# Kernel optimization log

Measured on AMD Instinct MI355X. Metric: run time of the kernel, lower is better.

## Reference

```python
import jax, jax.numpy as jnp
import numpy as np

PAD_IND = 3
SOS_IND = 0
NSTEPS = 25
H = 256   # hidden_size
D = 256   # input_size (embedding dim)
L = 3     # lstm_layers


def _lstm_cell(x, h, c, Wih, Whh, bih, bhh):
    # torch LSTM gate order: i, f, g, o
    g = x @ Wih.T + bih + h @ Whh.T + bhh
    i, f, gg, o = jnp.split(g, 4, axis=-1)
    c2 = jax.nn.sigmoid(f) * c + jax.nn.sigmoid(i) * jnp.tanh(gg)
    h2 = jax.nn.sigmoid(o) * jnp.tanh(c2)
    return h2, c2


def setup_inputs() -> dict:
    key = jax.random.key(0)
    ks = jax.random.split(key, 24)
    B, T = 64, 256
    Vin, C = 32000, 32000
    s = 1.0 / np.sqrt(H)

    def u(k, shape):
        return jax.random.uniform(k, shape, jnp.float32, -s, s)

    return dict(
        x=jax.random.randint(ks[0], (B, T), 0, Vin),
        target_val=jax.random.randint(ks[1], (B, NSTEPS), 0, C),
        enc_embed=jax.random.normal(ks[2], (Vin, D), jnp.float32),
        enc_Wih=u(ks[3], (L, 4 * H, D)),
        enc_Whh=u(ks[4], (L, 4 * H, H)),
        enc_bih=u(ks[5], (L, 4 * H)),
        enc_bhh=u(ks[6], (L, 4 * H)),
        Wq=u(ks[7], (H, H)), bq=u(ks[8], (H,)),
        Wk=u(ks[9], (H, H)), bk=u(ks[10], (H,)),
        Wv=u(ks[11], (H, H)), bv=u(ks[12], (H,)),
        Wo=u(ks[13], (H, H)), bo=u(ks[14], (H,)),
        dec_embed=jax.random.normal(ks[15], (C, D), jnp.float32),
        dec_Wih0=u(ks[16], (4 * H, 2 * H)),            # decoder layer 0 input is [emb; ctx] = 2H
        dec_Wih_rest=u(ks[17], (L - 1, 4 * H, H)),
        dec_Whh=u(ks[18], (L, 4 * H, H)),
        dec_bih=u(ks[19], (L, 4 * H)),
        dec_bhh=u(ks[20], (L, 4 * H)),
        dec_W=u(ks[21], (C, H)),
        dec_b=u(ks[22], (C,)),
    )


def reference(x, target_val, enc_embed, enc_Wih, enc_Whh, enc_bih, enc_bhh,
              Wq, bq, Wk, bk, Wv, bv, Wo, bo,
              dec_embed, dec_Wih0, dec_Wih_rest, dec_Whh, dec_bih, dec_bhh,
              dec_W, dec_b):
    B, T = x.shape
    lengths = (x != PAD_IND).sum(axis=1)            # [B], emulates pack_padded_sequence
    emb = enc_embed[x]                              # [B,T,D]
    valid = (jnp.arange(T)[:, None] < lengths[None, :])[..., None]  # [T,B,1]
    h0 = jnp.zeros((L, B, H), emb.dtype)
    c0 = jnp.zeros((L, B, H), emb.dtype)

    def enc_step(carry, inp):
        h, c = carry
        xt, v = inp
        hs, cs = [], []
        z = xt
        for l in range(L):
            hl, cl = _lstm_cell(z, h[l], c[l], enc_Wih[l], enc_Whh[l], enc_bih[l], enc_bhh[l])
            hl = jnp.where(v, hl, h[l])             # freeze state past sequence length
            cl = jnp.where(v, cl, c[l])
            hs.append(hl); cs.append(cl)
            z = hl
        h = jnp.stack(hs); c = jnp.stack(cs)
        return (h, c), jnp.where(v, h[-1], 0.0)     # pad_packed pads with zeros

    (enc_h, enc_c), outs = jax.lax.scan(enc_step, (h0, c0), (jnp.swapaxes(emb, 0, 1), valid))
    enc_hiddens = jnp.swapaxes(outs, 0, 1)          # [B,T,H]

    # attention key/value projections are loop-invariant -> hoist out of decode loop
    kp = enc_hiddens @ Wk.T + bk                    # [B,T,H]
    vp = enc_hiddens @ Wv.T + bv                    # [B,T,H]
    scale = 1.0 / jnp.sqrt(jnp.asarray(H, emb.dtype))
    dec_Wih = [dec_Wih0, dec_Wih_rest[0], dec_Wih_rest[1]]
    tok0 = jnp.full((B,), SOS_IND, jnp.int32)

    def dec_step(carry, _):
        h, c, tok = carry
        e = dec_embed[tok]                          # [B,D]
        q = h.sum(axis=0) @ Wq.T + bq               # prev_state[0].sum(axis=0) -> [B,H]
        scores = jnp.einsum('bh,bth->bt', q, kp) * scale
        attn = jax.nn.softmax(scores, axis=-1)
        ctx = jnp.einsum('bt,bth->bh', attn, vp) @ Wo.T + bo
        z = jnp.concatenate([e, ctx], axis=-1)      # [B,2H]
        hs, cs = [], []
        for l in range(L):
            hl, cl = _lstm_cell(z, h[l], c[l], dec_Wih[l], dec_Whh[l], dec_bih[l], dec_bhh[l])
            hs.append(hl); cs.append(cl)
            z = hl
        h = jnp.stack(hs); c = jnp.stack(cs)
        logits = z @ dec_W.T + dec_b                # [B,C]
        tok = jnp.argmax(logits, axis=-1).astype(jnp.int32)  # greedy feedback (TF ratio = 0)
        return (h, c, tok), logits

    _, logits = jax.lax.scan(dec_step, (enc_h, enc_c, tok0), None, length=NSTEPS)  # [25,B,C]
    return jnp.swapaxes(logits, 0, 1)[:, :, None, :]  # [B,25,1,C] like the torch module
```

## Files before the change

kernel.cpp:

```cpp
#include <hip/hip_runtime.h>
#include <math.h>

#define TT    256
#define NB    64
#define HH    256
#define NSTEP 25
#define NCLS  32000
#define PADI  3

__device__ __align__(16) float g_hring[3][2][NB][HH];
__device__ __align__(16) float g_enchid[TT][NB][HH];
__device__ __align__(16) float g_kp[NB][TT][HH];
__device__ __align__(16) float g_vp[NB][TT][HH];
__device__ __align__(16) float g_cfin[3][NB][HH];
__device__ __align__(16) float g_hdec[2][3][NB][HH];
__device__ __align__(16) float g_z0[NB][512];
__device__ float    g_wmax[256][NB];
__device__ int      g_wmaxi[256][NB];
__device__ int      g_len[NB];
__device__ unsigned g_arrive[256];
__device__ unsigned g_rel[256];

__global__ void k_zero_flags(){
  g_arrive[threadIdx.x] = 0u;
  g_rel[threadIdx.x] = 0u;
}

__device__ __forceinline__ float sigf(float v){ return 1.0f / (1.0f + expf(-v)); }

#define SCOPE_AG __HIP_MEMORY_SCOPE_AGENT
typedef unsigned long long u64;
__device__ __forceinline__ float2 ld2(const float* p){
  u64 v = __hip_atomic_load((const u64*)p, __ATOMIC_RELAXED, SCOPE_AG);
  float2 r; __builtin_memcpy(&r, &v, 8); return r;
}
__device__ __forceinline__ float ldc(const float* p){ return __hip_atomic_load(p, __ATOMIC_RELAXED, SCOPE_AG); }
__device__ __forceinline__ void  stc(float* p, float v){ __hip_atomic_store(p, v, __ATOMIC_RELAXED, SCOPE_AG); }
__device__ __forceinline__ int   ldi(const int* p){ return __hip_atomic_load(p, __ATOMIC_RELAXED, SCOPE_AG); }
__device__ __forceinline__ void  sti(int* p, int v){ __hip_atomic_store(p, v, __ATOMIC_RELAXED, SCOPE_AG); }
__device__ __forceinline__ unsigned ldu(const unsigned* p){ return __hip_atomic_load(p, __ATOMIC_RELAXED, SCOPE_AG); }
__device__ __forceinline__ void  stu(unsigned* p, unsigned v){ __hip_atomic_store(p, v, __ATOMIC_RELAXED, SCOPE_AG); }

#define DOT4(a_, x_, w_) (a_) += (x_).x*(w_).x + (x_).y*(w_).y + (x_).z*(w_).z + (x_).w*(w_).w

#define WENC(cb,g,jj,u) (((((cb)*12+(g))*8+(jj))*36)+(u))

__device__ __forceinline__ void gbar(int w, unsigned target){
  asm volatile("s_waitcnt vmcnt(0)" ::: "memory");
  __syncthreads();
  if (threadIdx.x == 0) stu(&g_arrive[w], target);
  if (w == 0){
    if (threadIdx.x < 64){
      const int i4 = threadIdx.x * 4;
      for (;;){
        unsigned a0 = ldu(&g_arrive[i4+0]);
        unsigned a1 = ldu(&g_arrive[i4+1]);
        unsigned a2 = ldu(&g_arrive[i4+2]);
        unsigned a3 = ldu(&g_arrive[i4+3]);
        if (__all((a0>=target) && (a1>=target) && (a2>=target) && (a3>=target))) break;
        __builtin_amdgcn_s_sleep(1);
      }
      if (threadIdx.x < 16) stu(&g_rel[threadIdx.x << 4], target);
    }
  } else {
    if (threadIdx.x == 0){
      const unsigned* line = &g_rel[(w >> 4) << 4];
      while (ldu(line) < target) __builtin_amdgcn_s_sleep(1);
    }
  }
  __syncthreads();
}

template<int NCB, int BASE>
__device__ __forceinline__ void dec_gates(const float* sw, const float* i0, const float* i1,
                                          const float* i2, int j, float out4[4]){
  float a0=0.f, a1=0.f, a2=0.f, a3=0.f;
  const float* ips[3] = { i0, i1, i2 };
  #pragma unroll
  for (int cb = 0; cb < NCB; ++cb){
    float2 xin[16];
    #pragma unroll
    for (int u = 0; u < 16; ++u) xin[u] = ld2(ips[cb] + u*16 + 2*j);
    #pragma unroll
    for (int u2 = 0; u2 < 8; ++u2){
      float2 pa = xin[2*u2], pb = xin[2*u2+1];
      const float* wb = &sw[BASE + (((cb*4+0)*8+j)*36) + u2*4];
      float4 w0 = *(const float4*)(wb);
      float4 w1 = *(const float4*)(wb + 288);
      float4 w2 = *(const float4*)(wb + 576);
      float4 w3 = *(const float4*)(wb + 864);
      a0 += pa.x*w0.x + pa.y*w0.y + pb.x*w0.z + pb.y*w0.w;
      a1 += pa.x*w1.x + pa.y*w1.y + pb.x*w1.z + pb.y*w1.w;
      a2 += pa.x*w2.x + pa.y*w2.y + pb.x*w2.z + pb.y*w2.w;
      a3 += pa.x*w3.x + pa.y*w3.y + pb.x*w3.z + pb.y*w3.w;
    }
  }
  #pragma unroll
  for (int m = 1; m < 8; m <<= 1){
    a0 += __shfl_xor(a0, m); a1 += __shfl_xor(a1, m);
    a2 += __shfl_xor(a2, m); a3 += __shfl_xor(a3, m);
  }
  out4[0]=a0; out4[1]=a1; out4[2]=a2; out4[3]=a3;
}

__global__ void __launch_bounds__(512, 1)
k_main(const int*   __restrict__ p_x,
       const float* __restrict__ p_eemb,
       const float* __restrict__ p_eWih,  const float* __restrict__ p_eWhh,
       const float* __restrict__ p_ebih,  const float* __restrict__ p_ebhh,
       const float* __restrict__ p_Wq, const float* __restrict__ p_bq,
       const float* __restrict__ p_Wk, const float* __restrict__ p_bk,
       const float* __restrict__ p_Wv, const float* __restrict__ p_bv,
       const float* __restrict__ p_Wo, const float* __restrict__ p_bo,
       const float* __restrict__ p_demb,
       const float* __restrict__ p_dWih0, const float* __restrict__ p_dWihR,
       const float* __restrict__ p_dWhh,
       const float* __restrict__ p_dbih,  const float* __restrict__ p_dbhh,
       const float* __restrict__ p_dW,    const float* __restrict__ p_db,
       float* __restrict__ p_out)
{
  __shared__ __align__(16) float s_w[8064];
  __shared__ __align__(16) float s_h2[NB*HH];
  __shared__ float s_benc[12];
  __shared__ float s_bdec[12];
  __shared__ __align__(16) float s_hs[256];
  __shared__ __align__(16) float s_q[256];
  __shared__ __align__(16) float s_sc[256];
  __shared__ __align__(16) float s_at[256];
  __shared__ __align__(16) float s_ctx[256];
  __shared__ float s_rv[8];  __shared__ int s_ri[8];

  const int w   = blockIdx.x;
  const int tid = threadIdx.x;
  const int b   = tid >> 3;
  const int j   = tid & 7;
  unsigned bar  = 0;

  const int lay0 = (w < 255) ? (w / 85) : 0;
  const int h0   = (w < 255) ? ((w - lay0*85) * 3) : 0;

  for (int fi = tid; fi < 6144; fi += 512){
    int g = fi >> 9, k = fi & 511;
    int e = g >> 2, gt = g & 3;
    int l   = (w < 255) ? lay0 : e;
    int hh2 = (w < 255) ? (h0 + e) : 255;
    int row = gt*256 + hh2;
    float v = (k < 256) ? p_eWih[((size_t)l*1024 + row)*256 + k]
                        : p_eWhh[((size_t)l*1024 + row)*256 + (k - 256)];
    int cb = k >> 8, kk = k & 255;
    s_w[WENC(cb, g, (kk & 15) >> 1, ((kk >> 4) << 1) | (kk & 1))] = v;
  }
  if (tid < 12){
    int e = tid >> 2, gt = tid & 3;
    int l   = (w < 255) ? lay0 : e;
    int hh2 = (w < 255) ? (h0 + e) : 255;
    int row = gt*256 + hh2;
    s_benc[tid] = p_ebih[l*1024 + row] + p_ebhh[l*1024 + row];
  }
  if (w < 64){
    int cnt = 0;
    if (tid < 256) cnt = (p_x[w*TT + tid] != PADI) ? 1 : 0;
    #pragma unroll
    for (int m = 1; m < 64; m <<= 1) cnt += __shfl_xor(cnt, m);
    if ((tid & 63) == 0) s_ri[tid >> 6] = cnt;
    __syncthreads();
    if (tid == 0){ int t2 = 0; for (int q2 = 0; q2 < 8; ++q2) t2 += s_ri[q2]; sti(&g_len[w], t2); }
  }
  if (tid < 192){
    int fi = w*192 + tid;
    int l = fi >> 14, rem = fi & 16383;
    stc(&g_hring[l][1][rem >> 8][rem & 255], 0.f);
  }
  gbar(w, ++bar);

  const int len_b = ldi(&g_len[b]);

  float c_reg[3] = {0.f,0.f,0.f};
  float h_reg[3] = {0.f,0.f,0.f};

  for (int sdiag = 0; sdiag < TT + 2; ++sdiag){
    float acc[12];
    #pragma unroll
    for (int g = 0; g < 12; ++g) acc[g] = 0.f;

    if (w < 255){
      const int t = sdiag - lay0;
      if (t >= 0 && t < TT){
        float2 x2[16], h2[16];
        if (lay0 == 0){
          const float* xs = p_eemb + (size_t)p_x[b*TT + t]*HH;
          #pragma unroll
          for (int u = 0; u < 16; ++u) x2[u] = *(const float2*)(xs + u*16 + 2*j);
        } else {
          const float* xs = &g_hring[lay0-1][t & 1][b][0];
          #pragma unroll
          for (int u = 0; u < 16; ++u) x2[u] = ld2(xs + u*16 + 2*j);
        }
        {
          const float* hsv = &g_hring[lay0][(t & 1) ^ 1][b][0];
          #pragma unroll
          for (int u = 0; u < 16; ++u) h2[u] = ld2(hsv + u*16 + 2*j);
        }
        #pragma unroll
        for (int u2 = 0; u2 < 8; ++u2){
          float2 xa = x2[2*u2], xb = x2[2*u2+1];
          float2 ha = h2[2*u2], hb = h2[2*u2+1];
          #pragma unroll
          for (int g = 0; g < 12; ++g){
            float4 wx = *(const float4*)&s_w[WENC(0, g, j, u2*4)];
            float4 wh = *(const float4*)&s_w[WENC(1, g, j, u2*4)];
            acc[g] += xa.x*wx.x + xa.y*wx.y + xb.x*wx.z + xb.y*wx.w
                    + ha.x*wh.x + ha.y*wh.y + hb.x*wh.z + hb.y*wh.w;
          }
        }
      }
    } else {
      #pragma unroll
      for (int e = 0; e < 3; ++e){
        const int t = sdiag - e;
        if (t >= 0 && t < TT){
          float2 x2[16], h2[16];
          if (e == 0){
            const float* xs = p_eemb + (size_t)p_x[b*TT + t]*HH;
            #pragma unroll
            for (int u = 0; u < 16; ++u) x2[u] = *(const float2*)(xs + u*16 + 2*j);
          } else {
            const float* xs = &g_hring[e-1][t & 1][b][0];
            #pragma unroll
            for (int u = 0; u < 16; ++u) x2[u] = ld2(xs + u*16 + 2*j);
          }
          {
            const float* hsv = &g_hring[e][(t & 1) ^ 1][b][0];
            #pragma unroll
            for (int u = 0; u < 16; ++u) h2[u] = ld2(hsv + u*16 + 2*j);
          }
          #pragma unroll
          for (int u2 = 0; u2 < 8; ++u2){
            float2 xa = x2[2*u2], xb = x2[2*u2+1];
            float2 ha = h2[2*u2], hb = h2[2*u2+1];
            #pragma unroll
            for (int g2 = 0; g2 < 4; ++g2){
              float4 wx = *(const float4*)&s_w[WENC(0, e*4+g2, j, u2*4)];
              float4 wh = *(const float4*)&s_w[WENC(1, e*4+g2, j, u2*4)];
              acc[e*4+g2] += xa.x*wx.x + xa.y*wx.y + xb.x*wx.z + xb.y*wx.w
                           + ha.x*wh.x + ha.y*wh.y + hb.x*wh.z + hb.y*wh.w;
            }
          }
        }
      }
    }

    #pragma unroll
    for (int g = 0; g < 12; ++g){
      float v = acc[g];
      v += __shfl_xor(v, 1); v += __shfl_xor(v, 2); v += __shfl_xor(v, 4);
      acc[g] = v;
    }

    if (j == 0){
      #pragma unroll
      for (int e = 0; e < 3; ++e){
        const int lay = (w < 255) ? lay0 : e;
        const int hh2 = (w < 255) ? (h0 + e) : 255;
        const int t = sdiag - lay;
        if (t >= 0 && t < TT){
          float iv = acc[e*4+0] + s_benc[e*4+0];
          float fv = acc[e*4+1] + s_benc[e*4+1];
          float gv = acc[e*4+2] + s_benc[e*4+2];
          float ov = acc[e*4+3] + s_benc[e*4+3];
          float c2 = sigf(fv)*c_reg[e] + sigf(iv)*tanhf(gv);
          float h2v = sigf(ov)*tanhf(c2);
          bool valid = (t < len_b);
          if (valid){ c_reg[e] = c2; h_reg[e] = h2v; }
          stc(&g_hring[lay][t & 1][b][hh2], h_reg[e]);
          if (lay == 2) stc(&g_enchid[t][b][hh2], valid ? h_reg[e] : 0.f);
        }
      }
    }
    gbar(w, ++bar);
  }

  if (j == 0){
    #pragma unroll
    for (int e = 0; e < 3; ++e){
      const int lay = (w < 255) ? lay0 : e;
      const int hh2 = (w < 255) ? (h0 + e) : 255;
      stc(&g_cfin[lay][b][hh2], c_reg[e]);
    }
  }
  gbar(w, ++bar);

  {
    const int b3 = w >> 2, t0 = (w & 3) * 64;
    const int n1 = tid & 127, rq = tid >> 7;
    for (int p = 0; p < 4; ++p){
      const int n = p*128 + n1;
      const float* wrow = (n < 256) ? (p_Wk + (size_t)n*HH) : (p_Wv + (size_t)(n-256)*HH);
      const float bias  = (n < 256) ? p_bk[n] : p_bv[n-256];
      const float4* wr4 = (const float4*)wrow;
      const float* hb = &g_enchid[t0 + rq*16][b3][0];
      const float4* hr[16];
      #pragma unroll
      for (int r = 0; r < 16; ++r) hr[r] = (const float4*)(hb + (size_t)r*NB*HH);
      float a16[16];
      #pragma unroll
      for (int r = 0; r < 16; ++r) a16[r] = 0.f;
      for (int k4 = 0; k4 < 64; ++k4){
        float4 wv = wr4[k4];
        #pragma unroll
        for (int r = 0; r < 16; ++r){ float4 h4 = hr[r][k4]; DOT4(a16[r], h4, wv); }
      }
      float* orow = (n < 256) ? &g_kp[b3][t0 + rq*16][n] : &g_vp[b3][t0 + rq*16][n-256];
      #pragma unroll
      for (int r = 0; r < 16; ++r) stc(orow + (size_t)r*HH, a16[r] + bias);
    }
  }

  for (int fi = tid; fi < 3072; fi += 512){
    int g = fi / 768, k = fi % 768; int row = g*256 + w;
    float v = (k < 512) ? p_dWih0[(size_t)row*512 + k]
                        : p_dWhh[(size_t)row*HH + (k - 512)];
    int cb = k >> 8, kk = k & 255;
    s_w[(((cb*4 + g)*8 + ((kk & 15) >> 1))*36) + (((kk >> 4) << 1) | (kk & 1))] = v;
  }
  for (int fi = tid; fi < 2048; fi += 512){
    int g = fi / 512, k = fi % 512; int row = g*256 + w;
    float v = (k < 256) ? p_dWihR[(size_t)row*HH + k]
                        : p_dWhh[(size_t)(1024 + row)*HH + (k - 256)];
    int cb = k >> 8, kk = k & 255;
    s_w[3456 + (((cb*4 + g)*8 + ((kk & 15) >> 1))*36) + (((kk >> 4) << 1) | (kk & 1))] = v;
  }
  for (int fi = tid; fi < 2048; fi += 512){
    int g = fi / 512, k = fi % 512; int row = g*256 + w;
    float v = (k < 256) ? p_dWihR[(size_t)(1024 + row)*HH + k]
                        : p_dWhh[(size_t)(2048 + row)*HH + (k - 256)];
    int cb = k >> 8, kk = k & 255;
    s_w[5760 + (((cb*4 + g)*8 + ((kk & 15) >> 1))*36) + (((kk >> 4) << 1) | (kk & 1))] = v;
  }
  if (tid < 12){
    int l = tid >> 2, g = tid & 3; int row = g*256 + w;
    s_bdec[tid] = p_dbih[l*1024 + row] + p_dbhh[l*1024 + row];
  }
  gbar(w, ++bar);

  if (tid < 192){
    int fi = w*192 + tid;
    int l = fi >> 14, rem = fi & 16383;
    stc(&g_hdec[0][l][rem >> 8][rem & 255], ldc(&g_hring[l][1][rem >> 8][rem & 255]));
  }
  float c_d0 = 0.f, c_d1 = 0.f, c_d2 = 0.f;
  if (j == 0){
    c_d0 = ldc(&g_cfin[0][b][w]); c_d1 = ldc(&g_cfin[1][b][w]); c_d2 = ldc(&g_cfin[2][b][w]);
  }
  gbar(w, ++bar);

  for (int st = 0; st < NSTEP; ++st){
    const int slot = st & 1, nxt = slot ^ 1;

    if (w < 64){
      const int bA = w;
      int tok = 0;
      if (st > 0){
        float v = -1e38f; int idx = 0;
        if (tid < 256){ v = ldc(&g_wmax[tid][bA]); idx = ldi(&g_wmaxi[tid][bA]); }
        #pragma unroll
        for (int m = 1; m < 64; m <<= 1){
          float ov = __shfl_xor(v, m); int oi = __shfl_xor(idx, m);
          if (ov > v || (ov == v && oi < idx)){ v = ov; idx = oi; }
        }
        if ((tid & 63) == 0){ s_rv[tid >> 6] = v; s_ri[tid >> 6] = idx; }
        __syncthreads();
        if (tid == 0){
          float bv2 = s_rv[0]; int bi2 = s_ri[0];
          for (int q2 = 1; q2 < 8; ++q2){
            float ov = s_rv[q2]; int oi = s_ri[q2];
            if (ov > bv2 || (ov == bv2 && oi < bi2)){ bv2 = ov; bi2 = oi; }
          }
          s_ri[0] = bi2;
        }
        __syncthreads();
        tok = s_ri[0];
      }
      if (tid < 256)
        s_hs[tid] = ldc(&g_hdec[slot][0][bA][tid]) + ldc(&g_hdec[slot][1][bA][tid])
                  + ldc(&g_hdec[slot][2][bA][tid]);
      __syncthreads();
      if (tid < 256){
        float a = p_bq[tid];
        const float4* wr = (const float4*)(p_Wq + (size_t)tid*HH);
        #pragma unroll 8
        for (int k4 = 0; k4 < 64; ++k4){
          float4 wv = wr[k4]; float4 h4 = *(const float4*)&s_hs[k4*4]; DOT4(a, h4, wv);
        }
        s_q[tid] = a;
      }
      __syncthreads();
      if (tid < 256){
        float a = 0.f;
        const float4* kr = (const float4*)&g_kp[bA][tid][0];
        #pragma unroll 8
        for (int k4 = 0; k4 < 64; ++k4){
          float4 kv = kr[k4]; float4 q4 = *(const float4*)&s_q[k4*4]; DOT4(a, q4, kv);
        }
        s_sc[tid] = a * 0.0625f;
      }
      __syncthreads();
      {
        float sv = (tid < 256) ? s_sc[tid] : -1e38f;
        float m2 = sv;
        #pragma unroll
        for (int m = 1; m < 64; m <<= 1) m2 = fmaxf(m2, __shfl_xor(m2, m));
        if ((tid & 63) == 0) s_rv[tid >> 6] = m2;
        __syncthreads();
        if (tid == 0){ float mm = s_rv[0]; for (int q2 = 1; q2 < 8; ++q2) mm = fmaxf(mm, s_rv[q2]); s_rv[0] = mm; }
        __syncthreads();
        const float mx = s_rv[0];
        float ev = (tid < 256) ? expf(sv - mx) : 0.f;
        float ss = ev;
        #pragma unroll
        for (int m = 1; m < 64; m <<= 1) ss += __shfl_xor(ss, m);
        __syncthreads();
        if ((tid & 63) == 0) s_rv[tid >> 6] = ss;
        __syncthreads();
        if (tid == 0){ float t2 = 0.f; for (int q2 = 0; q2 < 8; ++q2) t2 += s_rv[q2]; s_rv[0] = t2; }
        __syncthreads();
        if (tid < 256) s_at[tid] = ev / s_rv[0];
      }
      __syncthreads();
      if (tid < 256){
        float a = 0.f;
        const float* vb = &g_vp[bA][0][tid];
        #pragma unroll 4
        for (int t4 = 0; t4 < 64; ++t4){
          float4 a4 = *(const float4*)&s_at[t4*4];
          a += a4.x*vb[(size_t)(t4*4+0)*HH] + a4.y*vb[(size_t)(t4*4+1)*HH]
             + a4.z*vb[(size_t)(t4*4+2)*HH] + a4.w*vb[(size_t)(t4*4+3)*HH];
        }
        s_ctx[tid] = a;
      }
      __syncthreads();
      if (tid < 256){
        float a = p_bo[tid];
        const float4* wr = (const float4*)(p_Wo + (size_t)tid*HH);
        #pragma unroll 8
        for (int k4 = 0; k4 < 64; ++k4){
          float4 wv = wr[k4]; float4 c4 = *(const float4*)&s_ctx[k4*4]; DOT4(a, c4, wv);
        }
        stc(&g_z0[bA][256 + tid], a);
        stc(&g_z0[bA][tid], p_demb[(size_t)tok*HH + tid]);
      }
    }
    gbar(w, ++bar);

    {
      float g4[4];
      dec_gates<3, 0>(s_w, &g_z0[b][0], &g_z0[b][256], &g_hdec[slot][0][b][0], j, g4);
      if (j == 0){
        float iv = g4[0]+s_bdec[0], fv = g4[1]+s_bdec[1], gv = g4[2]+s_bdec[2], ov = g4[3]+s_bdec[3];
        float c2 = sigf(fv)*c_d0 + sigf(iv)*tanhf(gv); c_d0 = c2;
        stc(&g_hdec[nxt][0][b][w], sigf(ov)*tanhf(c2));
      }
    }
    gbar(w, ++bar);
    {
      float g4[4];
      dec_gates<2, 3456>(s_w, &g_hdec[nxt][0][b][0], &g_hdec[slot][1][b][0], nullptr, j, g4);
      if (j == 0){
        float iv = g4[0]+s_bdec[4], fv = g4[1]+s_bdec[5], gv = g4[2]+s_bdec[6], ov = g4[3]+s_bdec[7];
        float c2 = sigf(fv)*c_d1 + sigf(iv)*tanhf(gv); c_d1 = c2;
        stc(&g_hdec[nxt][1][b][w], sigf(ov)*tanhf(c2));
      }
    }
    gbar(w, ++bar);
    {
      float g4[4];
      dec_gates<2, 5760>(s_w, &g_hdec[nxt][1][b][0], &g_hdec[slot][2][b][0], nullptr, j, g4);
      if (j == 0){
        float iv = g4[0]+s_bdec[8], fv = g4[1]+s_bdec[9], gv = g4[2]+s_bdec[10], ov = g4[3]+s_bdec[11];
        float c2 = sigf(fv)*c_d2 + sigf(iv)*tanhf(gv); c_d2 = c2;
        stc(&g_hdec[nxt][2][b][w], sigf(ov)*tanhf(c2));
      }
    }
    gbar(w, ++bar);

    {
      {
        const float* src = &g_hdec[nxt][2][0][0];
        #pragma unroll
        for (int u = 0; u < 16; ++u){
          int fo = 2*(tid + 512*u);
          float2 v = ld2(src + fo);
          *(float2*)(s_h2 + fo) = v;
        }
      }
      __syncthreads();

      const int cs = tid & 63, qb = tid >> 6;
      const bool ok0 = (2*cs)   < 125;
      const bool ok1 = (2*cs+1) < 125;
      const int c0 = w*125 + 2*cs, c1 = c0 + 1;
      const float4* wr0 = (const float4*)(p_dW + (size_t)(ok0 ? c0 : w*125)*HH);
      const float4* wr1 = (const float4*)(p_dW + (size_t)(ok1 ? c1 : w*125)*HH);
      const float4* zr[8];
      #pragma unroll
      for (int r = 0; r < 8; ++r) zr[r] = (const float4*)&s_h2[(qb*8 + r)*HH];
      float a0[8], a1[8];
      #pragma unroll
      for (int r = 0; r < 8; ++r){ a0[r] = 0.f; a1[r] = 0.f; }
      for (int k4 = 0; k4 < 64; ++k4){
        float4 w0 = wr0[k4], w1 = wr1[k4];
        #pragma unroll
        for (int r = 0; r < 8; ++r){
          float4 z4 = zr[r][k4];
          DOT4(a0[r], z4, w0);
          DOT4(a1[r], z4, w1);
        }
      }
      const float bias0 = ok0 ? p_db[c0] : 0.f;
      const float bias1 = ok1 ? p_db[c1] : 0.f;
      #pragma unroll
      for (int r = 0; r < 8; ++r){
        const int bb = qb*8 + r;
        float val0 = a0[r] + bias0, val1 = a1[r] + bias1;
        float* orow = p_out + ((size_t)bb*NSTEP + st)*NCLS;
        if (ok0) orow[c0] = val0;
        if (ok1) orow[c1] = val1;
        float v = ok0 ? val0 : -1e38f;
        int idx  = ok0 ? c0 : 0x7fffffff;
        if (ok1 && val1 > v){ v = val1; idx = c1; }
        #pragma unroll
        for (int m = 1; m < 64; m <<= 1){
          float ov = __shfl_xor(v, m); int oi = __shfl_xor(idx, m);
          if (ov > v || (ov == v && oi < idx)){ v = ov; idx = oi; }
        }
        if (cs == 0){ stc(&g_wmax[w][bb], v); sti(&g_wmaxi[w][bb], idx); }
      }
    }
    gbar(w, ++bar);
  }
}

extern "C" void kernel_launch(void* const* d_in, const int* in_sizes, int n_in,
                              void* d_out, int out_size, void* d_ws, size_t ws_size,
                              hipStream_t stream){
  (void)in_sizes; (void)n_in; (void)out_size; (void)d_ws; (void)ws_size;
  const int*   x     = (const int*)d_in[0];
  const float* eemb  = (const float*)d_in[2];
  const float* eWih  = (const float*)d_in[3];
  const float* eWhh  = (const float*)d_in[4];
  const float* ebih  = (const float*)d_in[5];
  const float* ebhh  = (const float*)d_in[6];
  const float* Wq    = (const float*)d_in[7];
  const float* bq    = (const float*)d_in[8];
  const float* Wk    = (const float*)d_in[9];
  const float* bk    = (const float*)d_in[10];
  const float* Wv    = (const float*)d_in[11];
  const float* bv    = (const float*)d_in[12];
  const float* Wo    = (const float*)d_in[13];
  const float* bo    = (const float*)d_in[14];
  const float* demb  = (const float*)d_in[15];
  const float* dWih0 = (const float*)d_in[16];
  const float* dWihR = (const float*)d_in[17];
  const float* dWhh  = (const float*)d_in[18];
  const float* dbih  = (const float*)d_in[19];
  const float* dbhh  = (const float*)d_in[20];
  const float* dW    = (const float*)d_in[21];
  const float* db    = (const float*)d_in[22];
  float* out = (float*)d_out;

  k_zero_flags<<<dim3(1), dim3(256), 0, stream>>>();
  k_main<<<dim3(256), dim3(512), 0, stream>>>(
      x, eemb, eWih, eWhh, ebih, ebhh,
      Wq, bq, Wk, bk, Wv, bv, Wo, bo,
      demb, dWih0, dWihR, dWhh, dbih, dbhh, dW, db, out);
}
```

Measured before the change: 5.863 ms.

## Split encoder into dedicated kernel with per-layer local barriers and 4-deep ring

The encoder LSTM moves out of the monolithic persistent kernel into its own 192-block kernel, one 64-block group per layer. Each block computes 4 hidden units for all 64 batches and keeps its weights in shared memory. The 256-block grid barrier on every diagonal step is replaced by per-layer arrive/release flags. Each layer waits only on its own layer's previous step, the lower layer's current step, and the upper layer up to 4 steps behind, which a 4-slot h ring allows. Initialisation and length counting move into a separate init kernel. This aims to cut global-barrier latency and let layers run decoupled, at the cost of extra kernel launches and more complex flag-based synchronisation.

```diff
diff --git a/kernel.cpp b/kernel.cpp
--- a/kernel.cpp
+++ b/kernel.cpp
@@ -7,8 +7,9 @@
 #define NSTEP 25
 #define NCLS  32000
 #define PADI  3
-
-__device__ __align__(16) float g_hring[3][2][NB][HH];
+#define RING  4
+
+__device__ __align__(16) float g_hring[3][RING][NB][HH];
 __device__ __align__(16) float g_enchid[TT][NB][HH];
 __device__ __align__(16) float g_kp[NB][TT][HH];
 __device__ __align__(16) float g_vp[NB][TT][HH];
@@ -20,11 +21,8 @@
 __device__ int      g_len[NB];
 __device__ unsigned g_arrive[256];
 __device__ unsigned g_rel[256];
-
-__global__ void k_zero_flags(){
-  g_arrive[threadIdx.x] = 0u;
-  g_rel[threadIdx.x] = 0u;
-}
+__device__ unsigned g_earr[3][64];
+__device__ unsigned g_erel[3][64];
 
 __device__ __forceinline__ float sigf(float v){ return 1.0f / (1.0f + expf(-v)); }
 
@@ -43,7 +41,158 @@
 
 #define DOT4(a_, x_, w_) (a_) += (x_).x*(w_).x + (x_).y*(w_).y + (x_).z*(w_).z + (x_).w*(w_).w
 
-#define WENC(cb,g,jj,u) (((((cb)*12+(g))*8+(jj))*36)+(u))
+__global__ void __launch_bounds__(256) k_init(const int* __restrict__ p_x){
+  const int blk = blockIdx.x, tid = threadIdx.x;
+  if (blk < 192){
+    int idx = blk*256 + tid;
+    int l = idx >> 14, rem = idx & 16383;
+    g_hring[l][RING-1][rem >> 8][rem & 255] = 0.f;
+  } else {
+    __shared__ int s_c[4];
+    int b = blk - 192;
+    int cnt = (p_x[b*TT + tid] != PADI) ? 1 : 0;
+    #pragma unroll
+    for (int m = 1; m < 64; m <<= 1) cnt += __shfl_xor(cnt, m);
+    if ((tid & 63) == 0) s_c[tid >> 6] = cnt;
+    __syncthreads();
+    if (tid == 0) g_len[b] = s_c[0] + s_c[1] + s_c[2] + s_c[3];
+  }
+  if (blk == 0){ g_arrive[tid] = 0u; g_rel[tid] = 0u; }
+  if (blk == 1 && tid < 192){
+    ((unsigned*)g_earr)[tid] = 0u;
+    ((unsigned*)g_erel)[tid] = 0u;
+  }
+}
+
+__global__ void __launch_bounds__(512, 1)
+k_enc(const int*   __restrict__ p_x,
+      const float* __restrict__ p_eemb,
+      const float* __restrict__ p_eWih, const float* __restrict__ p_eWhh,
+      const float* __restrict__ p_ebih, const float* __restrict__ p_ebhh)
+{
+  __shared__ __align__(16) float s_W[8192];
+  __shared__ float s_gat[1024];
+  __shared__ float s_b[16];
+  __shared__ int   s_len[64];
+
+  const int w = blockIdx.x, tid = threadIdx.x;
+  const int l = w >> 6, q = w & 63;
+  const int b2 = tid >> 4, j = tid & 15;
+  const int ce = tid >> 6, cb = tid & 63;
+
+  for (int fi = tid; fi < 8192; fi += 512){
+    int row = fi >> 9, k = fi & 511;
+    int e = row >> 2, g = row & 3;
+    int wrow = g*256 + 4*q + e;
+    s_W[fi] = (k < 256) ? p_eWih[((size_t)l*1024 + wrow)*256 + k]
+                        : p_eWhh[((size_t)l*1024 + wrow)*256 + (k - 256)];
+  }
+  if (tid < 16){
+    int e = tid >> 2, g = tid & 3;
+    int wrow = g*256 + 4*q + e;
+    s_b[tid] = p_ebih[l*1024 + wrow] + p_ebhh[l*1024 + wrow];
+  }
+  if (tid < 64) s_len[tid] = g_len[tid];
+  float c_reg = 0.f, h_frz = 0.f;
+  __syncthreads();
+
+  for (int t = 0; t < TT; ++t){
+    if (tid == 0){
+      const int li = (q & 3) << 4;
+      for (;;){
+        bool ok = (ldu(&g_erel[l][li]) >= (unsigned)t);
+        if (ok && l > 0)          ok = (ldu(&g_erel[l-1][li]) >= (unsigned)(t+1));
+        if (ok && l < 2 && t >= 4) ok = (ldu(&g_erel[l+1][li]) >= (unsigned)(t-3));
+        if (ok) break;
+        __builtin_amdgcn_s_sleep(1);
+      }
+    }
+    __syncthreads();
+
+    float4 xin[2][4], hin[2][4];
+    #pragma unroll
+    for (int bb = 0; bb < 2; ++bb){
+      const int batch = 2*b2 + bb;
+      if (l == 0){
+        const float* xs = p_eemb + (size_t)p_x[batch*TT + t]*HH;
+        #pragma unroll
+        for (int u = 0; u < 4; ++u) xin[bb][u] = *(const float4*)(xs + u*64 + 4*j);
+      } else {
+        const float* xs = &g_hring[l-1][t & (RING-1)][batch][0];
+        #pragma unroll
+        for (int u = 0; u < 4; ++u){
+          float2 a = ld2(xs + u*64 + 4*j), c = ld2(xs + u*64 + 4*j + 2);
+          xin[bb][u] = make_float4(a.x, a.y, c.x, c.y);
+        }
+      }
+      const float* hs = &g_hring[l][(t + RING - 1) & (RING-1)][batch][0];
+      #pragma unroll
+      for (int u = 0; u < 4; ++u){
+        float2 a = ld2(hs + u*64 + 4*j), c = ld2(hs + u*64 + 4*j + 2);
+        hin[bb][u] = make_float4(a.x, a.y, c.x, c.y);
+      }
+    }
+
+    float acc[16][2];
+    #pragma unroll
+    for (int r = 0; r < 16; ++r){ acc[r][0] = 0.f; acc[r][1] = 0.f; }
+    #pragma unroll
+    for (int u = 0; u < 8; ++u){
+      float4 i0 = (u < 4) ? xin[0][u] : hin[0][u-4];
+      float4 i1 = (u < 4) ? xin[1][u] : hin[1][u-4];
+      #pragma unroll
+      for (int row = 0; row < 16; ++row){
+        float4 wv = *(const float4*)&s_W[row*512 + u*64 + 4*j];
+        DOT4(acc[row][0], i0, wv);
+        DOT4(acc[row][1], i1, wv);
+      }
+    }
+    #pragma unroll
+    for (int row = 0; row < 16; ++row){
+      #pragma unroll
+      for (int bb = 0; bb < 2; ++bb){
+        float v = acc[row][bb];
+        v += __shfl_xor(v, 1); v += __shfl_xor(v, 2);
+        v += __shfl_xor(v, 4); v += __shfl_xor(v, 8);
+        acc[row][bb] = v;
+      }
+    }
+    if (j == 0){
+      #pragma unroll
+      for (int row = 0; row < 16; ++row){
+        s_gat[row*64 + 2*b2    ] = acc[row][0];
+        s_gat[row*64 + 2*b2 + 1] = acc[row][1];
+      }
+    }
+    __syncthreads();
+
+    if (tid < 256){
+      float iv = s_gat[(ce*4+0)*64 + cb] + s_b[ce*4+0];
+      float fv = s_gat[(ce*4+1)*64 + cb] + s_b[ce*4+1];
+      float gv = s_gat[(ce*4+2)*64 + cb] + s_b[ce*4+2];
+      float ov = s_gat[(ce*4+3)*64 + cb] + s_b[ce*4+3];
+      float c2 = sigf(fv)*c_reg + sigf(iv)*tanhf(gv);
+      float h2 = sigf(ov)*tanhf(c2);
+      bool valid = (t < s_len[cb]);
+      if (valid) c_reg = c2;
+      h_frz = valid ? h2 : h_frz;
+      stc(&g_hring[l][t & (RING-1)][cb][4*q + ce], h_frz);
+      if (l == 2) g_enchid[t][cb][4*q + ce] = valid ? h_frz : 0.f;
+    }
+
+    asm volatile("s_waitcnt vmcnt(0)" ::: "memory");
+    __syncthreads();
+    if (tid == 0) stu(&g_earr[l][q], (unsigned)(t+1));
+    if (q == 0 && tid < 64){
+      while (!__all(ldu(&g_earr[l][tid]) >= (unsigned)(t+1)))
+        __builtin_amdgcn_s_sleep(1);
+      if (tid < 4) stu(&g_erel[l][tid << 4], (unsigned)(t+1));
+    }
+    __syncthreads();
+  }
+
+  if (tid < 256) g_cfin[l][cb][4*q + ce] = c_reg;
+}
 
 __device__ __forceinline__ void gbar(int w, unsigned target){
   asm volatile("s_waitcnt vmcnt(0)" ::: "memory");
@@ -104,24 +253,19 @@
 }
 
 __global__ void __launch_bounds__(512, 1)
-k_main(const int*   __restrict__ p_x,
-       const float* __restrict__ p_eemb,
-       const float* __restrict__ p_eWih,  const float* __restrict__ p_eWhh,
-       const float* __restrict__ p_ebih,  const float* __restrict__ p_ebhh,
-       const float* __restrict__ p_Wq, const float* __restrict__ p_bq,
-       const float* __restrict__ p_Wk, const float* __restrict__ p_bk,
-       const float* __restrict__ p_Wv, const float* __restrict__ p_bv,
-       const float* __restrict__ p_Wo, const float* __restrict__ p_bo,
-       const float* __restrict__ p_demb,
-       const float* __restrict__ p_dWih0, const float* __restrict__ p_dWihR,
-       const float* __restrict__ p_dWhh,
-       const float* __restrict__ p_dbih,  const float* __restrict__ p_dbhh,
-       const float* __restrict__ p_dW,    const float* __restrict__ p_db,
-       float* __restrict__ p_out)
+k_dec(const float* __restrict__ p_Wq, const float* __restrict__ p_bq,
+      const float* __restrict__ p_Wk, const float* __restrict__ p_bk,
+      const float* __restrict__ p_Wv, const float* __restrict__ p_bv,
+      const float* __restrict__ p_Wo, const float* __restrict__ p_bo,
+      const float* __restrict__ p_demb,
+      const float* __restrict__ p_dWih0, const float* __restrict__ p_dWihR,
+      const float* __restrict__ p_dWhh,
+      const float* __restrict__ p_dbih,  const float* __restrict__ p_dbhh,
+      const float* __restrict__ p_dW,    const float* __restrict__ p_db,
+      float* __restrict__ p_out)
 {
   __shared__ __align__(16) float s_w[8064];
   __shared__ __align__(16) float s_h2[NB*HH];
-  __shared__ float s_benc[12];
   __shared__ float s_bdec[12];
   __shared__ __align__(16) float s_hs[256];
   __shared__ __align__(16) float s_q[256];
@@ -135,160 +279,6 @@
   const int b   = tid >> 3;
   const int j   = tid & 7;
   unsigned bar  = 0;
-
-  const int lay0 = (w < 255) ? (w / 85) : 0;
-  const int h0   = (w < 255) ? ((w - lay0*85) * 3) : 0;
-
-  for (int fi = tid; fi < 6144; fi += 512){
-    int g = fi >> 9, k = fi & 511;
-    int e = g >> 2, gt = g & 3;
-    int l   = (w < 255) ? lay0 : e;
-    int hh2 = (w < 255) ? (h0 + e) : 255;
-    int row = gt*256 + hh2;
-    float v = (k < 256) ? p_eWih[((size_t)l*1024 + row)*256 + k]
-                        : p_eWhh[((size_t)l*1024 + row)*256 + (k - 256)];
-    int cb = k >> 8, kk = k & 255;
-    s_w[WENC(cb, g, (kk & 15) >> 1, ((kk >> 4) << 1) | (kk & 1))] = v;
-  }
-  if (tid < 12){
-    int e = tid >> 2, gt = tid & 3;
-    int l   = (w < 255) ? lay0 : e;
-    int hh2 = (w < 255) ? (h0 + e) : 255;
-    int row = gt*256 + hh2;
-    s_benc[tid] = p_ebih[l*1024 + row] + p_ebhh[l*1024 + row];
-  }
-  if (w < 64){
-    int cnt = 0;
-    if (tid < 256) cnt = (p_x[w*TT + tid] != PADI) ? 1 : 0;
-    #pragma unroll
-    for (int m = 1; m < 64; m <<= 1) cnt += __shfl_xor(cnt, m);
-    if ((tid & 63) == 0) s_ri[tid >> 6] = cnt;
-    __syncthreads();
-    if (tid == 0){ int t2 = 0; for (int q2 = 0; q2 < 8; ++q2) t2 += s_ri[q2]; sti(&g_len[w], t2); }
-  }
-  if (tid < 192){
-    int fi = w*192 + tid;
-    int l = fi >> 14, rem = fi & 16383;
-    stc(&g_hring[l][1][rem >> 8][rem & 255], 0.f);
-  }
-  gbar(w, ++bar);
-
-  const int len_b = ldi(&g_len[b]);
-
-  float c_reg[3] = {0.f,0.f,0.f};
-  float h_reg[3] = {0.f,0.f,0.f};
-
-  for (int sdiag = 0; sdiag < TT + 2; ++sdiag){
-    float acc[12];
-    #pragma unroll
-    for (int g = 0; g < 12; ++g) acc[g] = 0.f;
-
-    if (w < 255){
-      const int t = sdiag - lay0;
-      if (t >= 0 && t < TT){
-        float2 x2[16], h2[16];
-        if (lay0 == 0){
-          const float* xs = p_eemb + (size_t)p_x[b*TT + t]*HH;
-          #pragma unroll
-          for (int u = 0; u < 16; ++u) x2[u] = *(const float2*)(xs + u*16 + 2*j);
-        } else {
-          const float* xs = &g_hring[lay0-1][t & 1][b][0];
-          #pragma unroll
-          for (int u = 0; u < 16; ++u) x2[u] = ld2(xs + u*16 + 2*j);
-        }
-        {
-          const float* hsv = &g_hring[lay0][(t & 1) ^ 1][b][0];
-          #pragma unroll
-          for (int u = 0; u < 16; ++u) h2[u] = ld2(hsv + u*16 + 2*j);
-        }
-        #pragma unroll
-        for (int u2 = 0; u2 < 8; ++u2){
-          float2 xa = x2[2*u2], xb = x2[2*u2+1];
-          float2 ha = h2[2*u2], hb = h2[2*u2+1];
-          #pragma unroll
-          for (int g = 0; g < 12; ++g){
-            float4 wx = *(const float4*)&s_w[WENC(0, g, j, u2*4)];
-            float4 wh = *(const float4*)&s_w[WENC(1, g, j, u2*4)];
-            acc[g] += xa.x*wx.x + xa.y*wx.y + xb.x*wx.z + xb.y*wx.w
-                    + ha.x*wh.x + ha.y*wh.y + hb.x*wh.z + hb.y*wh.w;
-          }
-        }
-      }
-    } else {
-      #pragma unroll
-      for (int e = 0; e < 3; ++e){
-        const int t = sdiag - e;
-        if (t >= 0 && t < TT){
-          float2 x2[16], h2[16];
-          if (e == 0){
-            const float* xs = p_eemb + (size_t)p_x[b*TT + t]*HH;
-            #pragma unroll
-            for (int u = 0; u < 16; ++u) x2[u] = *(const float2*)(xs + u*16 + 2*j);
-          } else {
-            const float* xs = &g_hring[e-1][t & 1][b][0];
-            #pragma unroll
-            for (int u = 0; u < 16; ++u) x2[u] = ld2(xs + u*16 + 2*j);
-          }
-          {
-            const float* hsv = &g_hring[e][(t & 1) ^ 1][b][0];
-            #pragma unroll
-            for (int u = 0; u < 16; ++u) h2[u] = ld2(hsv + u*16 + 2*j);
-          }
-          #pragma unroll
-          for (int u2 = 0; u2 < 8; ++u2){
-            float2 xa = x2[2*u2], xb = x2[2*u2+1];
-            float2 ha = h2[2*u2], hb = h2[2*u2+1];
-            #pragma unroll
-            for (int g2 = 0; g2 < 4; ++g2){
-              float4 wx = *(const float4*)&s_w[WENC(0, e*4+g2, j, u2*4)];
-              float4 wh = *(const float4*)&s_w[WENC(1, e*4+g2, j, u2*4)];
-              acc[e*4+g2] += xa.x*wx.x + xa.y*wx.y + xb.x*wx.z + xb.y*wx.w
-                           + ha.x*wh.x + ha.y*wh.y + hb.x*wh.z + hb.y*wh.w;
-            }
-          }
-        }
-      }
-    }
-
-    #pragma unroll
-    for (int g = 0; g < 12; ++g){
-      float v = acc[g];
-      v += __shfl_xor(v, 1); v += __shfl_xor(v, 2); v += __shfl_xor(v, 4);
-      acc[g] = v;
-    }
-
-    if (j == 0){
-      #pragma unroll
-      for (int e = 0; e < 3; ++e){
-        const int lay = (w < 255) ? lay0 : e;
-        const int hh2 = (w < 255) ? (h0 + e) : 255;
-        const int t = sdiag - lay;
-        if (t >= 0 && t < TT){
-          float iv = acc[e*4+0] + s_benc[e*4+0];
-          float fv = acc[e*4+1] + s_benc[e*4+1];
-          float gv = acc[e*4+2] + s_benc[e*4+2];
-          float ov = acc[e*4+3] + s_benc[e*4+3];
-          float c2 = sigf(fv)*c_reg[e] + sigf(iv)*tanhf(gv);
-          float h2v = sigf(ov)*tanhf(c2);
-          bool valid = (t < len_b);
-          if (valid){ c_reg[e] = c2; h_reg[e] = h2v; }
-          stc(&g_hring[lay][t & 1][b][hh2], h_reg[e]);
-          if (lay == 2) stc(&g_enchid[t][b][hh2], valid ? h_reg[e] : 0.f);
-        }
-      }
-    }
-    gbar(w, ++bar);
-  }
-
-  if (j == 0){
-    #pragma unroll
-    for (int e = 0; e < 3; ++e){
-      const int lay = (w < 255) ? lay0 : e;
-      const int hh2 = (w < 255) ? (h0 + e) : 255;
-      stc(&g_cfin[lay][b][hh2], c_reg[e]);
-    }
-  }
-  gbar(w, ++bar);
 
   {
     const int b3 = w >> 2, t0 = (w & 3) * 64;
@@ -346,11 +336,11 @@
   if (tid < 192){
     int fi = w*192 + tid;
     int l = fi >> 14, rem = fi & 16383;
-    stc(&g_hdec[0][l][rem >> 8][rem & 255], ldc(&g_hring[l][1][rem >> 8][rem & 255]));
+    stc(&g_hdec[0][l][rem >> 8][rem & 255], ldc(&g_hring[l][RING-1][rem >> 8][rem & 255]));
   }
   float c_d0 = 0.f, c_d1 = 0.f, c_d2 = 0.f;
   if (j == 0){
-    c_d0 = ldc(&g_cfin[0][b][w]); c_d1 = ldc(&g_cfin[1][b][w]); c_d2 = ldc(&g_cfin[2][b][w]);
+    c_d0 = g_cfin[0][b][w]; c_d1 = g_cfin[1][b][w]; c_d2 = g_cfin[2][b][w];
   }
   gbar(w, ++bar);
 
@@ -568,9 +558,9 @@
   const float* db    = (const float*)d_in[22];
   float* out = (float*)d_out;
 
-  k_zero_flags<<<dim3(1), dim3(256), 0, stream>>>();
-  k_main<<<dim3(256), dim3(512), 0, stream>>>(
-      x, eemb, eWih, eWhh, ebih, ebhh,
-      Wq, bq, Wk, bk, Wv, bv, Wo, bo,
-      demb, dWih0, dWihR, dWhh, dbih, dbhh, dW, db, out);
-}
+  k_init<<<dim3(256), dim3(256), 0, stream>>>(x);
+  k_enc<<<dim3(192), dim3(512), 0, stream>>>(x, eemb, eWih, eWhh, ebih, ebhh);
+  k_dec<<<dim3(256), dim3(512), 0, stream>>>(Wq, bq, Wk, bk, Wv, bv, Wo, bo,
+                                             demb, dWih0, dWihR, dWhh, dbih, dbhh,
+                                             dW, db, out);
+}
```

Result: faster. 5.717 ms (-2.5%).
